# Optimization experiments

Hardware: AMD Instinct MI355X
Metric: run time of the kernel (lower is better)

The kernel has to match this reference:

```python
import jax, jax.numpy as jnp
import numpy as np

D_MODEL = 1024
HEADS = 16
D_HEAD = D_MODEL // HEADS


def setup_inputs() -> dict:
    key = jax.random.key(0)
    ks = jax.random.split(key, 7)
    s = 1.0 / np.sqrt(D_MODEL)
    x = jax.random.normal(ks[0], (4, 2048, D_MODEL), dtype=jnp.float32)
    Wq = jax.random.uniform(ks[1], (D_MODEL, D_MODEL), jnp.float32, -s, s)
    bq = jax.random.uniform(ks[2], (D_MODEL,), jnp.float32, -s, s)
    Wk = jax.random.uniform(ks[3], (D_MODEL, D_MODEL), jnp.float32, -s, s)
    bk = jax.random.uniform(ks[4], (D_MODEL,), jnp.float32, -s, s)
    Wv = jax.random.uniform(ks[5], (D_MODEL, D_MODEL), jnp.float32, -s, s)
    bv = jax.random.uniform(ks[6], (D_MODEL,), jnp.float32, -s, s)
    return {"x": x, "Wq": Wq, "bq": bq, "Wk": Wk, "bk": bk, "Wv": Wv, "bv": bv}


def reference(x, Wq, bq, Wk, bk, Wv, bv):
    B, S, D = x.shape
    # QKV projections, split heads: [B, H, S, Dh]
    def split(t):
        return t.reshape(B, S, HEADS, D_HEAD).transpose(0, 2, 1, 3)
    q = split(x @ Wq + bq)
    k = split(x @ Wk + bk)
    v = split(x @ Wv + bv)
    scores = jnp.einsum('bhqd,bhkd->bhqk', q, k) / np.sqrt(D_HEAD).astype(jnp.float32)
    attn = jax.nn.softmax(scores, axis=-1)
    out = jnp.einsum('bhqk,bhkd->bhqd', attn, v)
    return out.transpose(0, 2, 1, 3).reshape(B, S, D)
```

## Files before the change

kernel.cpp:

```cpp
#include <hip/hip_runtime.h>

typedef _Float16 f16;
typedef __attribute__((ext_vector_type(2))) _Float16 f16x2;
typedef __attribute__((ext_vector_type(2))) __fp16   hf16x2;
typedef __attribute__((ext_vector_type(4))) _Float16 f16x4;
typedef __attribute__((ext_vector_type(8))) _Float16 f16x8;
typedef __attribute__((ext_vector_type(4))) float    f32x4;

#define D_MODEL 1024
#define HEADS   16
#define DH      64
#define SEQ     2048
#define BATCH   4
#define SSCALE  0.1803368801111204f

__device__ __forceinline__ void gload_lds16(const void* g, void* lds) {
  __builtin_amdgcn_global_load_lds(
      (const __attribute__((address_space(1))) unsigned int*)g,
      (__attribute__((address_space(3))) unsigned int*)lds, 16, 0, 0);
}

__global__ __launch_bounds__(256) void prep_kernel(const float* __restrict__ x,
                                                   const float* __restrict__ Wq,
                                                   const float* __restrict__ Wk,
                                                   const float* __restrict__ Wv,
                                                   f16* __restrict__ xb,
                                                   f16* __restrict__ wt) {
  if (blockIdx.x < 8192) {
    int i = blockIdx.x * 256 + threadIdx.x;
    float4 v = ((const float4*)x)[i];
    f16x4 h;
    h[0] = (f16)v.x; h[1] = (f16)v.y; h[2] = (f16)v.z; h[3] = (f16)v.w;
    ((f16x4*)xb)[i] = h;
    return;
  }
  int bid = blockIdx.x - 8192;
  int z = bid >> 8, rem = bid & 255;
  const float* W = z == 0 ? Wq : (z == 1 ? Wk : Wv);
  f16* out = wt + (size_t)z * D_MODEL * D_MODEL;
  __shared__ float tile[64][65];
  int n0 = (rem & 15) * 64, k0 = (rem >> 4) * 64;
  int tx = threadIdx.x & 63, ty = threadIdx.x >> 6;
#pragma unroll
  for (int r = 0; r < 16; ++r)
    tile[ty * 16 + r][tx] = W[(size_t)(k0 + ty * 16 + r) * D_MODEL + n0 + tx];
  __syncthreads();
#pragma unroll
  for (int r = 0; r < 16; ++r)
    out[(size_t)(n0 + ty * 16 + r) * D_MODEL + k0 + tx] = (f16)tile[tx][ty * 16 + r];
}

__global__ __launch_bounds__(256, 3) void qkv_gemm_kernel(
    const f16* __restrict__ xb, const f16* __restrict__ wt_all,
    const float* __restrict__ bq, const float* __restrict__ bk, const float* __restrict__ bv,
    f16* __restrict__ qout, f16* __restrict__ kout, f16* __restrict__ vtout) {
  const int bid = blockIdx.x;
  const int j = bid & 7, t = bid >> 3;
  const int by = j * 8 + (t & 7);
  const int bx = (t >> 3) & 7;
  const int z  = t >> 6;
  const f16* wt = wt_all + (size_t)z * D_MODEL * D_MODEL;
  const float* bias = z == 0 ? bq : (z == 1 ? bk : bv);
  const int n0 = bx * 128, m0 = by * 128;

  __shared__ f16 As[3][128 * 32];
  __shared__ f16 Bs[3][128 * 32];

  const int tid = threadIdx.x;
  const int lane = tid & 63, w = tid >> 6;
  const int quad = lane >> 4, l15 = lane & 15;
  const int wm = w & 1, wn = w >> 1;

  const int pce = (quad ^ ((l15 >> 1) & 3)) * 8;
  const int aoff = wm * 2048 + l15 * 32 + pce;
  const int boff = wn * 2048 + l15 * 32 + pce;

  int srow[2], scl[2];
#pragma unroll
  for (int c = 0; c < 2; ++c) {
    int slot = (w * 2 + c) * 64 + lane;
    srow[c] = slot >> 2;
    scl[c] = (slot & 3) ^ ((srow[c] >> 1) & 3);
  }

  f32x4 acc[4][4];
#pragma unroll
  for (int i = 0; i < 4; ++i)
#pragma unroll
    for (int jj = 0; jj < 4; ++jj) acc[i][jj] = (f32x4){0.f, 0.f, 0.f, 0.f};

#pragma unroll
  for (int tt = 0; tt < 2; ++tt)
#pragma unroll
    for (int c = 0; c < 2; ++c) {
      gload_lds16(xb + (size_t)(m0 + srow[c]) * D_MODEL + tt * 32 + scl[c] * 8, &As[tt][(w * 2 + c) * 512]);
      gload_lds16(wt + (size_t)(n0 + srow[c]) * D_MODEL + tt * 32 + scl[c] * 8, &Bs[tt][(w * 2 + c) * 512]);
    }

  f16x8 aP[4], bP[4];
  int buf = 0;
  for (int it = 0; it < 32; ++it) {
    if (it == 31) { asm volatile("s_waitcnt vmcnt(0)" ::: "memory"); }
    else          { asm volatile("s_waitcnt vmcnt(4)" ::: "memory"); }
    __builtin_amdgcn_s_barrier();
    __builtin_amdgcn_sched_barrier(0);
    if (it < 30) {
      const int sb = buf ? buf - 1 : 2;
      const int kn = (it + 2) * 32;
#pragma unroll
      for (int c = 0; c < 2; ++c) {
        gload_lds16(xb + (size_t)(m0 + srow[c]) * D_MODEL + kn + scl[c] * 8, &As[sb][(w * 2 + c) * 512]);
        gload_lds16(wt + (size_t)(n0 + srow[c]) * D_MODEL + kn + scl[c] * 8, &Bs[sb][(w * 2 + c) * 512]);
      }
    }
    f16x8 aC[4], bC[4];
#pragma unroll
    for (int mt = 0; mt < 4; ++mt) aC[mt] = *(const f16x8*)(&As[buf][aoff + mt * 512]);
#pragma unroll
    for (int nt = 0; nt < 4; ++nt) bC[nt] = *(const f16x8*)(&Bs[buf][boff + nt * 512]);
    if (it) {
#pragma unroll
      for (int mt = 0; mt < 4; ++mt)
#pragma unroll
        for (int nt = 0; nt < 4; ++nt)
          acc[mt][nt] = __builtin_amdgcn_mfma_f32_16x16x32_f16(aP[mt], bP[nt], acc[mt][nt], 0, 0, 0);
    }
#pragma unroll
    for (int tt = 0; tt < 4; ++tt) { aP[tt] = aC[tt]; bP[tt] = bC[tt]; }
    buf = (buf == 2) ? 0 : buf + 1;
  }
#pragma unroll
  for (int mt = 0; mt < 4; ++mt)
#pragma unroll
    for (int nt = 0; nt < 4; ++nt)
      acc[mt][nt] = __builtin_amdgcn_mfma_f32_16x16x32_f16(aP[mt], bP[nt], acc[mt][nt], 0, 0, 0);

  const float sc = (z == 0) ? SSCALE : 1.0f;
  float bcol[4];
#pragma unroll
  for (int nt = 0; nt < 4; ++nt) bcol[nt] = bias[n0 + wn * 64 + nt * 16 + l15];

  if (z < 2) {
    f16* out = (z == 0) ? qout : kout;
#pragma unroll
    for (int mt = 0; mt < 4; ++mt) {
      int mbase = m0 + wm * 64 + mt * 16 + quad * 4;
#pragma unroll
      for (int nt = 0; nt < 4; ++nt) {
        int n = n0 + wn * 64 + nt * 16 + l15;
        int h = n >> 6, dh = n & 63;
#pragma unroll
        for (int r = 0; r < 4; ++r) {
          int m = mbase + r;
          int b = m >> 11, s = m & 2047;
          out[((size_t)(b * HEADS + h) * SEQ + s) * DH + dh] = (f16)((acc[mt][nt][r] + bcol[nt]) * sc);
        }
      }
    }
  } else {
#pragma unroll
    for (int mt = 0; mt < 4; ++mt) {
      int mbase = m0 + wm * 64 + mt * 16 + quad * 4;
      int b = mbase >> 11, seq = mbase & 2047;
      int kt = seq >> 6;
#pragma unroll
      for (int nt = 0; nt < 4; ++nt) {
        int n = n0 + wn * 64 + nt * 16 + l15;
        int h = n >> 6, dh = n & 63;
        f16x4 v;
#pragma unroll
        for (int r = 0; r < 4; ++r) v[r] = (f16)(acc[mt][nt][r] + bcol[nt]);
        int phys = (quad * 2 + (mt >> 1)) ^ (dh & 7);
        size_t off = (((size_t)(b * HEADS + h) * 32 + kt) * 4096) + dh * 64 + phys * 8 + (mt & 1) * 4;
        *(f16x4*)(vtout + off) = v;
      }
    }
  }
}

__global__ __launch_bounds__(256, 2) void attn_kernel(
    const f16* __restrict__ q, const f16* __restrict__ k, const f16* __restrict__ vt,
    float* __restrict__ out) {
  const int bh = blockIdx.x;
  const int s0 = blockIdx.y * 256;
  const int b = bh >> 4, h = bh & 15;
  const int tid = threadIdx.x, lane = tid & 63, w = tid >> 6;
  const int quad = lane >> 4, l15 = lane & 15;

  __shared__ f16 Ks[3][64 * 64];
  __shared__ f16 Vs[3][64 * 64];

  const f16* qbase = q + ((size_t)bh * SEQ + s0 + w * 64) * DH;
  const f16* kbase = k + (size_t)bh * SEQ * DH;
  const f16* vbase = vt + (size_t)bh * DH * SEQ;

  f16x8 qf[4][2];
#pragma unroll
  for (int qt = 0; qt < 4; ++qt)
#pragma unroll
    for (int ks = 0; ks < 2; ++ks)
      qf[qt][ks] = *(const f16x8*)(qbase + (qt * 16 + l15) * DH + ks * 32 + quad * 8);

  int koff[2];
  koff[0] = l15 * 64 + ((quad ^ (l15 & 7)) * 8);
  koff[1] = l15 * 64 + (((4 + quad) ^ (l15 & 7)) * 8);
  int voff2[2];
  voff2[0] = l15 * 64 + (((quad * 2) ^ (l15 & 7)) * 8);
  voff2[1] = l15 * 64 + (((quad * 2 + 1) ^ (l15 & 7)) * 8);

  int srow[2], scl[2];
#pragma unroll
  for (int c = 0; c < 2; ++c) {
    int slot = (w * 2 + c) * 64 + lane;
    srow[c] = slot >> 3;
    scl[c] = (slot & 7) ^ (srow[c] & 7);
  }
  const int vslot = ((w * 2) * 64 + lane) * 8;
  const int vslot2 = ((w * 2 + 1) * 64 + lane) * 8;

  f32x4 lsum4[4];
#pragma unroll
  for (int qt = 0; qt < 4; ++qt) lsum4[qt] = (f32x4){0.f, 0.f, 0.f, 0.f};
  f32x4 o[4][4];
#pragma unroll
  for (int i = 0; i < 4; ++i)
#pragma unroll
    for (int jj = 0; jj < 4; ++jj) o[i][jj] = (f32x4){0.f, 0.f, 0.f, 0.f};
  const f32x4 Zero = (f32x4){0.f, 0.f, 0.f, 0.f};

#pragma unroll
  for (int t = 0; t < 2; ++t) {
#pragma unroll
    for (int c = 0; c < 2; ++c)
      gload_lds16(kbase + (size_t)(t * 64 + srow[c]) * DH + scl[c] * 8, &Ks[t][(w * 2 + c) * 512]);
    gload_lds16(vbase + t * 4096 + vslot,  &Vs[t][(w * 2) * 512]);
    gload_lds16(vbase + t * 4096 + vslot2, &Vs[t][(w * 2 + 1) * 512]);
  }

  int buf = 0;
  for (int kt = 0; kt < SEQ / 64; ++kt) {
    if (kt == SEQ / 64 - 1) { asm volatile("s_waitcnt vmcnt(0)" ::: "memory"); }
    else                    { asm volatile("s_waitcnt vmcnt(4)" ::: "memory"); }
    __builtin_amdgcn_s_barrier();
    __builtin_amdgcn_sched_barrier(0);
    if (kt < SEQ / 64 - 2) {
      const int sb = buf ? buf - 1 : 2;
      const int kn = (kt + 2) * 64;
#pragma unroll
      for (int c = 0; c < 2; ++c)
        gload_lds16(kbase + (size_t)(kn + srow[c]) * DH + scl[c] * 8, &Ks[sb][(w * 2 + c) * 512]);
      gload_lds16(vbase + (kt + 2) * 4096 + vslot,  &Vs[sb][(w * 2) * 512]);
      gload_lds16(vbase + (kt + 2) * 4096 + vslot2, &Vs[sb][(w * 2 + 1) * 512]);
    }

    f32x4 st[4][4];
#pragma unroll
    for (int mt = 0; mt < 4; ++mt) {
      f16x8 af0 = *(const f16x8*)(&Ks[buf][koff[0] + mt * 1024]);
      f16x8 af1 = *(const f16x8*)(&Ks[buf][koff[1] + mt * 1024]);
#pragma unroll
      for (int qt = 0; qt < 4; ++qt) {
        st[mt][qt] = __builtin_amdgcn_mfma_f32_16x16x32_f16(af0, qf[qt][0], Zero, 0, 0, 0);
        st[mt][qt] = __builtin_amdgcn_mfma_f32_16x16x32_f16(af1, qf[qt][1], st[mt][qt], 0, 0, 0);
      }
    }

    f16x4 pb[4][4];
#pragma unroll
    for (int ks = 0; ks < 4; ++ks)
#pragma unroll
      for (int qt = 0; qt < 4; ++qt) {
        float e0 = __builtin_amdgcn_exp2f(st[ks][qt][0]);
        float e1 = __builtin_amdgcn_exp2f(st[ks][qt][1]);
        float e2 = __builtin_amdgcn_exp2f(st[ks][qt][2]);
        float e3 = __builtin_amdgcn_exp2f(st[ks][qt][3]);
        f32x4 ev = (f32x4){e0, e1, e2, e3};
        lsum4[qt] += ev;
        f16x2 p01 = __builtin_bit_cast(f16x2, __builtin_amdgcn_cvt_pkrtz(e0, e1));
        f16x2 p23 = __builtin_bit_cast(f16x2, __builtin_amdgcn_cvt_pkrtz(e2, e3));
        pb[ks][qt] = __builtin_shufflevector(p01, p23, 0, 1, 2, 3);
      }

#pragma unroll
    for (int half = 0; half < 2; ++half)
#pragma unroll
      for (int mt = 0; mt < 4; ++mt) {
        f16x8 v8 = *(const f16x8*)(&Vs[buf][voff2[half] + mt * 1024]);
        f16x4 vaA = __builtin_shufflevector(v8, v8, 0, 1, 2, 3);
        f16x4 vaB = __builtin_shufflevector(v8, v8, 4, 5, 6, 7);
#pragma unroll
        for (int qt = 0; qt < 4; ++qt) {
          o[mt][qt] = __builtin_amdgcn_mfma_f32_16x16x16f16(vaA, pb[half * 2][qt], o[mt][qt], 0, 0, 0);
          o[mt][qt] = __builtin_amdgcn_mfma_f32_16x16x16f16(vaB, pb[half * 2 + 1][qt], o[mt][qt], 0, 0, 0);
        }
      }
    buf = (buf == 2) ? 0 : buf + 1;
  }

#pragma unroll
  for (int qt = 0; qt < 4; ++qt) {
    float l = (lsum4[qt][0] + lsum4[qt][1]) + (lsum4[qt][2] + lsum4[qt][3]);
    l += __shfl_xor(l, 16, 64);
    l += __shfl_xor(l, 32, 64);
    float inv = 1.f / l;
    int sq = s0 + w * 64 + qt * 16 + l15;
    float* obase = out + ((size_t)b * SEQ + sq) * D_MODEL + h * DH;
#pragma unroll
    for (int mt = 0; mt < 4; ++mt) {
      f32x4 vv;
#pragma unroll
      for (int r = 0; r < 4; ++r) vv[r] = o[mt][qt][r] * inv;
      *(f32x4*)(obase + mt * 16 + quad * 4) = vv;
    }
  }
}

extern "C" void kernel_launch(void* const* d_in, const int* in_sizes, int n_in,
                              void* d_out, int out_size, void* d_ws, size_t ws_size,
                              hipStream_t stream) {
  const float* x  = (const float*)d_in[0];
  const float* Wq = (const float*)d_in[1];
  const float* bq = (const float*)d_in[2];
  const float* Wk = (const float*)d_in[3];
  const float* bk = (const float*)d_in[4];
  const float* Wv = (const float*)d_in[5];
  const float* bv = (const float*)d_in[6];
  float* out = (float*)d_out;

  char* ws = (char*)d_ws;
  f16* xb = (f16*)ws;
  f16* wt = (f16*)(ws + (size_t)16 * 1024 * 1024);
  f16* q  = (f16*)(ws + (size_t)22 * 1024 * 1024);
  f16* kk = q + (size_t)BATCH * SEQ * D_MODEL;
  f16* vt = kk + (size_t)BATCH * SEQ * D_MODEL;

  prep_kernel<<<8192 + 768, 256, 0, stream>>>(x, Wq, Wk, Wv, xb, wt);
  qkv_gemm_kernel<<<1536, 256, 0, stream>>>(xb, wt, bq, bk, bv, q, kk, vt);
  attn_kernel<<<dim3(64, 8), 256, 0, stream>>>(q, kk, vt, out);
}
```

Before: 245.8 us.

## Software-pipeline QK^T of next key tile with softmax and PV of current tile

Restructures the attention inner loop so that the QK^T MFMAs for key tile kt+1 are issued interleaved with the exp/convert and PV MFMAs of tile kt. Two score buffers ping-pong across a manually unrolled-by-two loop. The manual vmcnt waits are replaced by __syncthreads, and staging is factored into a lambda. The aim is to hide exp latency and the MFMA dependency chains behind independent matrix work. The cost is roughly 64 more accumulator registers, which may hurt occupancy. The full-drain barrier may also reduce the effective prefetch depth.

```diff
diff --git a/kernel.cpp b/kernel.cpp
--- a/kernel.cpp
+++ b/kernel.cpp
@@ -218,6 +218,14 @@
   const int vslot = ((w * 2) * 64 + lane) * 8;
   const int vslot2 = ((w * 2 + 1) * 64 + lane) * 8;
 
+  auto stage = [&](int t, int rs) {
+#pragma unroll
+    for (int c = 0; c < 2; ++c)
+      gload_lds16(kbase + (size_t)(t * 64 + srow[c]) * DH + scl[c] * 8, &Ks[rs][(w * 2 + c) * 512]);
+    gload_lds16(vbase + (size_t)t * 4096 + vslot,  &Vs[rs][(w * 2) * 512]);
+    gload_lds16(vbase + (size_t)t * 4096 + vslot2, &Vs[rs][(w * 2 + 1) * 512]);
+  };
+
   f32x4 lsum4[4];
 #pragma unroll
   for (int qt = 0; qt < 4; ++qt) lsum4[qt] = (f32x4){0.f, 0.f, 0.f, 0.f};
@@ -228,73 +236,73 @@
     for (int jj = 0; jj < 4; ++jj) o[i][jj] = (f32x4){0.f, 0.f, 0.f, 0.f};
   const f32x4 Zero = (f32x4){0.f, 0.f, 0.f, 0.f};
 
-#pragma unroll
-  for (int t = 0; t < 2; ++t) {
-#pragma unroll
-    for (int c = 0; c < 2; ++c)
-      gload_lds16(kbase + (size_t)(t * 64 + srow[c]) * DH + scl[c] * 8, &Ks[t][(w * 2 + c) * 512]);
-    gload_lds16(vbase + t * 4096 + vslot,  &Vs[t][(w * 2) * 512]);
-    gload_lds16(vbase + t * 4096 + vslot2, &Vs[t][(w * 2 + 1) * 512]);
-  }
-
-  int buf = 0;
-  for (int kt = 0; kt < SEQ / 64; ++kt) {
-    if (kt == SEQ / 64 - 1) { asm volatile("s_waitcnt vmcnt(0)" ::: "memory"); }
-    else                    { asm volatile("s_waitcnt vmcnt(4)" ::: "memory"); }
-    __builtin_amdgcn_s_barrier();
-    __builtin_amdgcn_sched_barrier(0);
-    if (kt < SEQ / 64 - 2) {
-      const int sb = buf ? buf - 1 : 2;
-      const int kn = (kt + 2) * 64;
-#pragma unroll
-      for (int c = 0; c < 2; ++c)
-        gload_lds16(kbase + (size_t)(kn + srow[c]) * DH + scl[c] * 8, &Ks[sb][(w * 2 + c) * 512]);
-      gload_lds16(vbase + (kt + 2) * 4096 + vslot,  &Vs[sb][(w * 2) * 512]);
-      gload_lds16(vbase + (kt + 2) * 4096 + vslot2, &Vs[sb][(w * 2 + 1) * 512]);
-    }
-
-    f32x4 st[4][4];
+  stage(0, 0);
+  stage(1, 1);
+  __syncthreads();
+
+  f32x4 stA[4][4], stB[4][4];
+#pragma unroll
+  for (int mt = 0; mt < 4; ++mt) {
+    f16x8 af0 = *(const f16x8*)(&Ks[0][koff[0] + mt * 1024]);
+    f16x8 af1 = *(const f16x8*)(&Ks[0][koff[1] + mt * 1024]);
+#pragma unroll
+    for (int qt = 0; qt < 4; ++qt) {
+      stA[mt][qt] = __builtin_amdgcn_mfma_f32_16x16x32_f16(af0, qf[qt][0], Zero, 0, 0, 0);
+      stA[mt][qt] = __builtin_amdgcn_mfma_f32_16x16x32_f16(af1, qf[qt][1], stA[mt][qt], 0, 0, 0);
+    }
+  }
+
+  int rc = 0;
+  auto step = [&](int kt, f32x4 (&stOld)[4][4], f32x4 (&stNew)[4][4]) {
+    __syncthreads();
+    const int rn = (rc == 2) ? 0 : rc + 1;
+    if (kt < 30) {
+      const int rs = rc ? rc - 1 : 2;
+      stage(kt + 2, rs);
+    }
+    f16x4 pb[4][4];
 #pragma unroll
     for (int mt = 0; mt < 4; ++mt) {
-      f16x8 af0 = *(const f16x8*)(&Ks[buf][koff[0] + mt * 1024]);
-      f16x8 af1 = *(const f16x8*)(&Ks[buf][koff[1] + mt * 1024]);
 #pragma unroll
       for (int qt = 0; qt < 4; ++qt) {
-        st[mt][qt] = __builtin_amdgcn_mfma_f32_16x16x32_f16(af0, qf[qt][0], Zero, 0, 0, 0);
-        st[mt][qt] = __builtin_amdgcn_mfma_f32_16x16x32_f16(af1, qf[qt][1], st[mt][qt], 0, 0, 0);
-      }
-    }
-
-    f16x4 pb[4][4];
-#pragma unroll
-    for (int ks = 0; ks < 4; ++ks)
-#pragma unroll
-      for (int qt = 0; qt < 4; ++qt) {
-        float e0 = __builtin_amdgcn_exp2f(st[ks][qt][0]);
-        float e1 = __builtin_amdgcn_exp2f(st[ks][qt][1]);
-        float e2 = __builtin_amdgcn_exp2f(st[ks][qt][2]);
-        float e3 = __builtin_amdgcn_exp2f(st[ks][qt][3]);
-        f32x4 ev = (f32x4){e0, e1, e2, e3};
-        lsum4[qt] += ev;
+        float e0 = __builtin_amdgcn_exp2f(stOld[mt][qt][0]);
+        float e1 = __builtin_amdgcn_exp2f(stOld[mt][qt][1]);
+        float e2 = __builtin_amdgcn_exp2f(stOld[mt][qt][2]);
+        float e3 = __builtin_amdgcn_exp2f(stOld[mt][qt][3]);
+        lsum4[qt] += (f32x4){e0, e1, e2, e3};
         f16x2 p01 = __builtin_bit_cast(f16x2, __builtin_amdgcn_cvt_pkrtz(e0, e1));
         f16x2 p23 = __builtin_bit_cast(f16x2, __builtin_amdgcn_cvt_pkrtz(e2, e3));
-        pb[ks][qt] = __builtin_shufflevector(p01, p23, 0, 1, 2, 3);
-      }
-
+        pb[mt][qt] = __builtin_shufflevector(p01, p23, 0, 1, 2, 3);
+      }
+      if (kt < 31) {
+        f16x8 af0 = *(const f16x8*)(&Ks[rn][koff[0] + mt * 1024]);
+        f16x8 af1 = *(const f16x8*)(&Ks[rn][koff[1] + mt * 1024]);
+#pragma unroll
+        for (int qt = 0; qt < 4; ++qt) {
+          stNew[mt][qt] = __builtin_amdgcn_mfma_f32_16x16x32_f16(af0, qf[qt][0], Zero, 0, 0, 0);
+          stNew[mt][qt] = __builtin_amdgcn_mfma_f32_16x16x32_f16(af1, qf[qt][1], stNew[mt][qt], 0, 0, 0);
+        }
+      }
+    }
 #pragma unroll
     for (int half = 0; half < 2; ++half)
 #pragma unroll
-      for (int mt = 0; mt < 4; ++mt) {
-        f16x8 v8 = *(const f16x8*)(&Vs[buf][voff2[half] + mt * 1024]);
+      for (int mtv = 0; mtv < 4; ++mtv) {
+        f16x8 v8 = *(const f16x8*)(&Vs[rc][voff2[half] + mtv * 1024]);
         f16x4 vaA = __builtin_shufflevector(v8, v8, 0, 1, 2, 3);
         f16x4 vaB = __builtin_shufflevector(v8, v8, 4, 5, 6, 7);
 #pragma unroll
         for (int qt = 0; qt < 4; ++qt) {
-          o[mt][qt] = __builtin_amdgcn_mfma_f32_16x16x16f16(vaA, pb[half * 2][qt], o[mt][qt], 0, 0, 0);
-          o[mt][qt] = __builtin_amdgcn_mfma_f32_16x16x16f16(vaB, pb[half * 2 + 1][qt], o[mt][qt], 0, 0, 0);
+          o[mtv][qt] = __builtin_amdgcn_mfma_f32_16x16x16f16(vaA, pb[half * 2][qt], o[mtv][qt], 0, 0, 0);
+          o[mtv][qt] = __builtin_amdgcn_mfma_f32_16x16x16f16(vaB, pb[half * 2 + 1][qt], o[mtv][qt], 0, 0, 0);
         }
       }
-    buf = (buf == 2) ? 0 : buf + 1;
+    rc = rn;
+  };
+
+  for (int ih = 0; ih < 16; ++ih) {
+    step(2 * ih,     stA, stB);
+    step(2 * ih + 1, stB, stA);
   }
 
 #pragma unroll
```

Result: slower. 259.4 us (+5.5%).
